# Kernel optimization log

Hardware: AMD Instinct MI355X
Metric: run time of the kernel (lower is better)

The kernel has to match this reference:

```python
import jax, jax.numpy as jnp
import numpy as np

N = 100000   # particles
D = 100      # grid cells per dimension


def setup_inputs() -> dict:
    rng = np.random.default_rng(0)
    d = 0.05  # cell_size in source
    # distinct cells (module assumes one particle per cell)
    cells = rng.choice(D ** 3, size=N, replace=False)
    cz = cells // (D * D)
    cy = (cells // D) % D
    cx = cells % D
    jit = rng.uniform(-0.3, 0.3, size=(3, N)) * d  # |jitter| < 0.5*d keeps round(pos/d)==cell
    x = cx * d + jit[0]
    y = cy * d + jit[1]
    z = cz * d + jit[2]
    v = rng.standard_normal((3, N)) * 0.1
    kn = 60000.0
    restitution = 0.5
    alpha = -np.log(restitution) / np.pi
    gamma = alpha / np.sqrt(alpha ** 2 + 1.0)
    rho_p = 2700.0
    particle_mass = 4.0 / 3.0 * 3.1415 * d ** 3 * rho_p
    eta = 2.0 * gamma * np.sqrt(kn * particle_mass / 2.0)
    return {
        "compressed_x_grid": jnp.asarray(x, jnp.float32),
        "compressed_y_grid": jnp.asarray(y, jnp.float32),
        "compressed_z_grid": jnp.asarray(z, jnp.float32),
        "compressed_vx_grid": jnp.asarray(v[0], jnp.float32),
        "compressed_vy_grid": jnp.asarray(v[1], jnp.float32),
        "compressed_vz_grid": jnp.asarray(v[2], jnp.float32),
        "d": float(d),
        "kn": float(kn),
        "damping_coefficient_Eta": float(eta),
        "friction_coefficient": 0.5,
        "dt": 0.001,
        "input_shape": D,
        "filter_size": 5,
    }


def _forces(x, y, z, vx, vy, vz, d, kn, eta, grid_dim, filter_size):
    n = x.shape[0]
    eps = 1e-4
    # cell indices exactly as in the torch code: round(pos/d)
    cx = jnp.round(x / d).astype(jnp.int32)
    cy = jnp.round(y / d).astype(jnp.int32)
    cz = jnp.round(z / d).astype(jnp.int32)
    # dense particle-index grid; -1 = empty (replaces mask + particle_number_tensor)
    idx = -jnp.ones((grid_dim, grid_dim, grid_dim), jnp.int32)
    idx = idx.at[cz, cy, cx].set(jnp.arange(n, dtype=jnp.int32))
    # all filter_size^3 roll offsets; torch.roll wraps, so use modular indexing
    r = filter_size // 2
    ar = jnp.arange(-r, r + 1)
    off = jnp.stack(jnp.meshgrid(ar, ar, ar, indexing="ij"), axis=-1).reshape(-1, 3)  # [K,3] (sz,sy,sx)
    # pair (A at cell c) with (B at cell c - s): mask_contact_A==2 <=> occ[c] & occ[c-s]
    nz = (cz[:, None] - off[None, :, 0]) % grid_dim  # [N,K]
    ny = (cy[:, None] - off[None, :, 1]) % grid_dim
    nx = (cx[:, None] - off[None, :, 2]) % grid_dim
    B = idx[nz, ny, nx]                                   # [N,K] neighbor particle id or -1
    me = jnp.arange(n, dtype=jnp.int32)[:, None]
    valid = (B >= 0) & (B != me)                          # filters empty cells and self pairs (A != B)
    Bs = jnp.where(valid, B, 0)
    dxp = x[:, None] - x[Bs]
    dyp = y[:, None] - y[Bs]
    dzp = z[:, None] - z[Bs]
    dvx = vx[:, None] - vx[Bs]
    dvy = vy[:, None] - vy[Bs]
    dvz = vz[:, None] - vz[Bs]
    dist = jnp.sqrt(dxp * dxp + dyp * dyp + dzp * dzp)
    denom = jnp.maximum(eps, dist)
    contact = valid & (dist < 2.0 * d)
    # spring (collision) force on A, aggregated over neighbors (row-sum == scatter_add to A)
    coef = jnp.where(contact, kn * (dist - 2.0 * d) / denom, 0.0)
    fx_c = (coef * dxp).sum(axis=1)
    fy_c = (coef * dyp).sum(axis=1)
    fz_c = (coef * dzp).sum(axis=1)
    # normal damping force
    vn = (dvx * dxp + dvy * dyp + dvz * dzp) / denom
    dcoef = jnp.where(contact, eta * vn / denom, 0.0)
    fx_d = (dcoef * dxp).sum(axis=1)
    fy_d = (dcoef * dyp).sum(axis=1)
    fz_d = (dcoef * dzp).sum(axis=1)
    return jnp.stack([fx_c, fy_c, fz_c, fx_d, fy_d, fz_d])  # [6, N]


def reference(compressed_x_grid, compressed_y_grid, compressed_z_grid, compressed_vx_grid, compressed_vy_grid, compressed_vz_grid, d, kn, damping_coefficient_Eta, friction_coefficient, dt, input_shape, filter_size):
    return _forces(compressed_x_grid, compressed_y_grid, compressed_z_grid,
                   compressed_vx_grid, compressed_vy_grid, compressed_vz_grid,
                   d, kn, damping_coefficient_Eta, input_shape, filter_size)
```

## Files before the change

kernel.cpp:

```cpp
#include <hip/hip_runtime.h>

static const int DG = 100;
static const int PGD = DG + 4;
static const int PCELLS = PGD * PGD * PGD;

static const int TX = 10, TY = 10, TZ = 5;
static const int HX = TX + 4, HY = TY + 4, HZ = TZ + 4;
static const int HPLANE = HX * HY;
static const int HCELLS = HPLANE * HZ;
static const int TCELLS = TX * TY * TZ;
static const int NTX = DG / TX, NTY = DG / TY, NTZ = DG / TZ;
static const int NTILES = NTX * NTY * NTZ;

static const int BLK = 512;


__global__ __launch_bounds__(256) void scatter_kernel(
    const float* __restrict__ x, const float* __restrict__ y, const float* __restrict__ z,
    const float* __restrict__ vx, const float* __restrict__ vy, const float* __restrict__ vz,
    const float* __restrict__ dptr,
    float4* __restrict__ posid, float4* __restrict__ vel4, int n)
{
    int i = blockIdx.x * blockDim.x + threadIdx.x;
    if (i >= n) return;
    float inv_d = 1.0f / dptr[0];
    float xi = x[i], yi = y[i], zi = z[i];
    int cx = (int)roundf(xi * inv_d);
    int cy = (int)roundf(yi * inv_d);
    int cz = (int)roundf(zi * inv_d);
    int cell = ((cz + 2) * PGD + (cy + 2)) * PGD + (cx + 2);
    float4 pv;
    pv.x = xi; pv.y = yi; pv.z = zi; pv.w = __int_as_float(i);
    posid[cell] = pv;
    float4 vv;
    vv.x = vx[i]; vv.y = vy[i]; vv.z = vz[i]; vv.w = 0.0f;
    vel4[i] = vv;
}

__global__ __launch_bounds__(BLK) void force_kernel(
    const float* __restrict__ dptr, const float* __restrict__ knptr,
    const float* __restrict__ etaptr,
    const float4* __restrict__ posid, const float4* __restrict__ vel4,
    float* __restrict__ out, int n)
{
    __shared__ float4 tile[HCELLS];
    __shared__ unsigned short list[TCELLS];
    __shared__ int cnt;

    int b = blockIdx.x;
    int txi = b % NTX;
    int tyi = (b / NTX) % NTY;
    int tzi = b / (NTX * NTY);
    int ox = txi * TX, oy = tyi * TY, oz = tzi * TZ;

    int t = threadIdx.x;
    if (t == 0) cnt = 0;

    for (int l = t; l < HCELLS; l += BLK) {
        int lz = l / HPLANE;
        int r  = l - lz * HPLANE;
        int ly = r / HX;
        int lx = r - ly * HX;
        tile[l] = posid[((oz + lz) * PGD + (oy + ly)) * PGD + (ox + lx)];
    }
    __syncthreads();

    if (t < TCELLS) {
        int iz = t / (TX * TY);
        int r  = t - iz * (TX * TY);
        int iy = r / TX;
        int ix = r - iy * TX;
        int l = (iz + 2) * HPLANE + (iy + 2) * HX + (ix + 2);
        if (__float_as_int(tile[l].w) >= 0) {
            int pos = atomicAdd(&cnt, 1);
            list[pos] = (unsigned short)l;
        }
    }
    __syncthreads();
    int nOcc = cnt;
    if (nOcc == 0) return;

    float d   = dptr[0];
    float kn  = knptr[0];
    float eta = etaptr[0];
    float two_d = 2.0f * d;

    int lane = t & 63;
    int wv   = t >> 6;
    int sub  = lane >> 4;
    int l16  = lane & 15;

    int offs[8];
    #pragma unroll
    for (int j = 0; j < 8; ++j) {
        int k = l16 + 16 * j;
        if (k > 124) k = 62;
        int sz = k / 25; int rr = k - sz * 25; int sy = rr / 5; int sx = rr - sy * 5;
        offs[j] = (sz - 2) * HPLANE + (sy - 2) * HX + (sx - 2);
    }

    int nRounds = (nOcc + 31) >> 5;
    for (int rd = 0; rd < nRounds; ++rd) {
        int iw = rd * 32 + wv * 4 + sub;
        bool active = (iw < nOcc);
        int il = active ? iw : (nOcc - 1);
        int c = list[il];
        float4 self = tile[c];
        int pid = __float_as_int(self.w);
        float4 pvel = vel4[pid];

        float fxc = 0.f, fyc = 0.f, fzc = 0.f;
        float fxd = 0.f, fyd = 0.f, fzd = 0.f;
        unsigned int cmask = 0;

        #pragma unroll
        for (int j = 0; j < 8; ++j) {
            float4 nb = tile[c + offs[j]];
            int B = __float_as_int(nb.w);
            bool valid = (B >= 0) & (B != pid);
            float nx = valid ? nb.x : self.x;
            float ny = valid ? nb.y : self.y;
            float nz = valid ? nb.z : self.z;
            float dxp = self.x - nx;
            float dyp = self.y - ny;
            float dzp = self.z - nz;
            float d2 = dxp * dxp + dyp * dyp + dzp * dzp;
            float dist = __builtin_amdgcn_sqrtf(d2);
            bool contact = valid & (dist < two_d);
            float denom   = fmaxf(1e-4f, dist);
            float inv_den = __builtin_amdgcn_rcpf(denom);
            float coef = contact ? kn * (dist - two_d) * inv_den : 0.0f;
            fxc += coef * dxp; fyc += coef * dyp; fzc += coef * dzp;
            cmask |= (contact ? 1u : 0u) << j;
        }

        while (__builtin_amdgcn_ballot_w64(cmask != 0)) {
            if (cmask) {
                int j = __builtin_ctz(cmask);
                cmask &= cmask - 1;
                float4 nb = tile[c + offs[j]];
                int B = __float_as_int(nb.w);
                float dxp = self.x - nb.x;
                float dyp = self.y - nb.y;
                float dzp = self.z - nb.z;
                float d2 = dxp * dxp + dyp * dyp + dzp * dzp;
                float dist = __builtin_amdgcn_sqrtf(d2);
                float denom   = fmaxf(1e-4f, dist);
                float inv_den = __builtin_amdgcn_rcpf(denom);
                float4 bv = vel4[B];
                float dvxp = pvel.x - bv.x;
                float dvyp = pvel.y - bv.y;
                float dvzp = pvel.z - bv.z;
                float vn    = (dvxp * dxp + dvyp * dyp + dvzp * dzp) * inv_den;
                float dcoef = eta * vn * inv_den;
                fxd += dcoef * dxp; fyd += dcoef * dyp; fzd += dcoef * dzp;
            }
        }

        #pragma unroll
        for (int off = 8; off >= 1; off >>= 1) {
            fxc += __shfl_xor(fxc, off, 16);
            fyc += __shfl_xor(fyc, off, 16);
            fzc += __shfl_xor(fzc, off, 16);
            fxd += __shfl_xor(fxd, off, 16);
            fyd += __shfl_xor(fyd, off, 16);
            fzd += __shfl_xor(fzd, off, 16);
        }

        if (active && l16 < 6) {
            float v = (l16 == 0) ? fxc
                    : (l16 == 1) ? fyc
                    : (l16 == 2) ? fzc
                    : (l16 == 3) ? fxd
                    : (l16 == 4) ? fyd : fzd;
            out[l16 * n + pid] = v;
        }
    }
}

extern "C" void kernel_launch(void* const* d_in, const int* in_sizes, int n_in,
                              void* d_out, int out_size, void* d_ws, size_t ws_size,
                              hipStream_t stream)
{
    const float* x     = (const float*)d_in[0];
    const float* y     = (const float*)d_in[1];
    const float* z     = (const float*)d_in[2];
    const float* vx    = (const float*)d_in[3];
    const float* vy    = (const float*)d_in[4];
    const float* vz    = (const float*)d_in[5];
    const float* dptr  = (const float*)d_in[6];
    const float* knptr = (const float*)d_in[7];
    const float* etap  = (const float*)d_in[8];
    int n = in_sizes[0];

    float4* posid = (float4*)d_ws;
    float4* vel4  = (float4*)((char*)d_ws + (size_t)PCELLS * sizeof(float4));

    hipMemsetAsync(posid, 0xFF, (size_t)PCELLS * sizeof(float4), stream);

    int sblocks = (n + 255) / 256;
    scatter_kernel<<<sblocks, 256, 0, stream>>>(x, y, z, vx, vy, vz, dptr,
                                                posid, vel4, n);

    force_kernel<<<NTILES, BLK, 0, stream>>>(dptr, knptr, etap,
                                             posid, vel4, (float*)d_out, n);
}
```

Before: 119.9 us.

## Pack grid cells into 8-byte quantized cell-relative positions plus particle id

Each grid cell changes from a float4 (absolute position plus id) to a uint2 holding a 17-bit particle id and 15-bit fixed-point offsets within the cell. The force kernel rebuilds pair displacements from integer cell offsets and quantized fractions. This halves the memset, scatter and tile-load traffic and the shared-memory footprint. The cost is some bit unpacking, a loss of position precision to about d/32768, and a limit of 2^17 particles.

```diff
diff --git a/kernel.cpp b/kernel.cpp
--- a/kernel.cpp
+++ b/kernel.cpp
@@ -19,7 +19,7 @@
     const float* __restrict__ x, const float* __restrict__ y, const float* __restrict__ z,
     const float* __restrict__ vx, const float* __restrict__ vy, const float* __restrict__ vz,
     const float* __restrict__ dptr,
-    float4* __restrict__ posid, float4* __restrict__ vel4, int n)
+    uint2* __restrict__ grid, float4* __restrict__ vel4, int n)
 {
     int i = blockIdx.x * blockDim.x + threadIdx.x;
     if (i >= n) return;
@@ -28,10 +28,13 @@
     int cx = (int)roundf(xi * inv_d);
     int cy = (int)roundf(yi * inv_d);
     int cz = (int)roundf(zi * inv_d);
-    int cell = ((cz + 2) * PGD + (cy + 2)) * PGD + (cx + 2);
-    float4 pv;
-    pv.x = xi; pv.y = yi; pv.z = zi; pv.w = __int_as_float(i);
-    posid[cell] = pv;
+    unsigned qx = (unsigned)__float2int_rn((xi * inv_d - (float)cx + 0.5f) * 32768.0f);
+    unsigned qy = (unsigned)__float2int_rn((yi * inv_d - (float)cy + 0.5f) * 32768.0f);
+    unsigned qz = (unsigned)__float2int_rn((zi * inv_d - (float)cz + 0.5f) * 32768.0f);
+    uint2 w;
+    w.x = (unsigned)i | (qx << 17);
+    w.y = qy | (qz << 15);
+    grid[((cz + 2) * PGD + (cy + 2)) * PGD + (cx + 2)] = w;
     float4 vv;
     vv.x = vx[i]; vv.y = vy[i]; vv.z = vz[i]; vv.w = 0.0f;
     vel4[i] = vv;
@@ -40,10 +43,10 @@
 __global__ __launch_bounds__(BLK) void force_kernel(
     const float* __restrict__ dptr, const float* __restrict__ knptr,
     const float* __restrict__ etaptr,
-    const float4* __restrict__ posid, const float4* __restrict__ vel4,
+    const uint2* __restrict__ grid, const float4* __restrict__ vel4,
     float* __restrict__ out, int n)
 {
-    __shared__ float4 tile[HCELLS];
+    __shared__ uint2 tile[HCELLS];
     __shared__ unsigned short list[TCELLS];
     __shared__ int cnt;
 
@@ -61,7 +64,7 @@
         int r  = l - lz * HPLANE;
         int ly = r / HX;
         int lx = r - ly * HX;
-        tile[l] = posid[((oz + lz) * PGD + (oy + ly)) * PGD + (ox + lx)];
+        tile[l] = grid[((oz + lz) * PGD + (oy + ly)) * PGD + (ox + lx)];
     }
     __syncthreads();
 
@@ -71,7 +74,7 @@
         int iy = r / TX;
         int ix = r - iy * TX;
         int l = (iz + 2) * HPLANE + (iy + 2) * HX + (ix + 2);
-        if (__float_as_int(tile[l].w) >= 0) {
+        if (tile[l].x != 0xFFFFFFFFu) {
             int pos = atomicAdd(&cnt, 1);
             list[pos] = (unsigned short)l;
         }
@@ -83,20 +86,24 @@
     float d   = dptr[0];
     float kn  = knptr[0];
     float eta = etaptr[0];
-    float two_d = 2.0f * d;
+    float two_d  = 2.0f * d;
+    float dscale = d * (1.0f / 32768.0f);
 
     int lane = t & 63;
     int wv   = t >> 6;
     int sub  = lane >> 4;
     int l16  = lane & 15;
 
-    int offs[8];
+    int offs[8], i0x[8], i0y[8], i0z[8];
     #pragma unroll
     for (int j = 0; j < 8; ++j) {
         int k = l16 + 16 * j;
         if (k > 124) k = 62;
         int sz = k / 25; int rr = k - sz * 25; int sy = rr / 5; int sx = rr - sy * 5;
         offs[j] = (sz - 2) * HPLANE + (sy - 2) * HX + (sx - 2);
+        i0x[j] = (2 - sx) << 15;
+        i0y[j] = (2 - sy) << 15;
+        i0z[j] = (2 - sz) << 15;
     }
 
     int nRounds = (nOcc + 31) >> 5;
@@ -105,8 +112,11 @@
         bool active = (iw < nOcc);
         int il = active ? iw : (nOcc - 1);
         int c = list[il];
-        float4 self = tile[c];
-        int pid = __float_as_int(self.w);
+        uint2 sw = tile[c];
+        int pid = (int)(sw.x & 0x1FFFFu);
+        int sqx = (int)(sw.x >> 17);
+        int sqy = (int)(sw.y & 0x7FFFu);
+        int sqz = (int)((sw.y >> 15) & 0x7FFFu);
         float4 pvel = vel4[pid];
 
         float fxc = 0.f, fyc = 0.f, fzc = 0.f;
@@ -115,15 +125,15 @@
 
         #pragma unroll
         for (int j = 0; j < 8; ++j) {
-            float4 nb = tile[c + offs[j]];
-            int B = __float_as_int(nb.w);
-            bool valid = (B >= 0) & (B != pid);
-            float nx = valid ? nb.x : self.x;
-            float ny = valid ? nb.y : self.y;
-            float nz = valid ? nb.z : self.z;
-            float dxp = self.x - nx;
-            float dyp = self.y - ny;
-            float dzp = self.z - nz;
+            uint2 nb = tile[c + offs[j]];
+            int id  = (int)(nb.x & 0x1FFFFu);
+            bool valid = (nb.x != 0xFFFFFFFFu) & (id != pid);
+            int nqx = (int)(nb.x >> 17);
+            int nqy = (int)(nb.y & 0x7FFFu);
+            int nqz = (int)((nb.y >> 15) & 0x7FFFu);
+            float dxp = (float)(i0x[j] + sqx - nqx) * dscale;
+            float dyp = (float)(i0y[j] + sqy - nqy) * dscale;
+            float dzp = (float)(i0z[j] + sqz - nqz) * dscale;
             float d2 = dxp * dxp + dyp * dyp + dzp * dzp;
             float dist = __builtin_amdgcn_sqrtf(d2);
             bool contact = valid & (dist < two_d);
@@ -138,11 +148,14 @@
             if (cmask) {
                 int j = __builtin_ctz(cmask);
                 cmask &= cmask - 1;
-                float4 nb = tile[c + offs[j]];
-                int B = __float_as_int(nb.w);
-                float dxp = self.x - nb.x;
-                float dyp = self.y - nb.y;
-                float dzp = self.z - nb.z;
+                uint2 nb = tile[c + offs[j]];
+                int B   = (int)(nb.x & 0x1FFFFu);
+                int nqx = (int)(nb.x >> 17);
+                int nqy = (int)(nb.y & 0x7FFFu);
+                int nqz = (int)((nb.y >> 15) & 0x7FFFu);
+                float dxp = (float)(i0x[j] + sqx - nqx) * dscale;
+                float dyp = (float)(i0y[j] + sqy - nqy) * dscale;
+                float dzp = (float)(i0z[j] + sqz - nqz) * dscale;
                 float d2 = dxp * dxp + dyp * dyp + dzp * dzp;
                 float dist = __builtin_amdgcn_sqrtf(d2);
                 float denom   = fmaxf(1e-4f, dist);
@@ -193,15 +206,15 @@
     const float* etap  = (const float*)d_in[8];
     int n = in_sizes[0];
 
-    float4* posid = (float4*)d_ws;
-    float4* vel4  = (float4*)((char*)d_ws + (size_t)PCELLS * sizeof(float4));
-
-    hipMemsetAsync(posid, 0xFF, (size_t)PCELLS * sizeof(float4), stream);
+    uint2*  grid = (uint2*)d_ws;
+    float4* vel4 = (float4*)((char*)d_ws + (size_t)PCELLS * sizeof(uint2));
+
+    hipMemsetAsync(grid, 0xFF, (size_t)PCELLS * sizeof(uint2), stream);
 
     int sblocks = (n + 255) / 256;
     scatter_kernel<<<sblocks, 256, 0, stream>>>(x, y, z, vx, vy, vz, dptr,
-                                                posid, vel4, n);
+                                                grid, vel4, n);
 
     force_kernel<<<NTILES, BLK, 0, stream>>>(dptr, knptr, etap,
-                                             posid, vel4, (float*)d_out, n);
+                                             grid, vel4, (float*)d_out, n);
 }
```

After: 126.8 us. 1.06x slower.
